# Optimization experiments

Hardware: AMD Instinct MI355X
Metric: run time of the kernel (lower is better)

The kernel has to match this reference:

```python
import jax, jax.numpy as jnp
from jax import lax
import numpy as np

_B, _D, _H, _W = 4, 32, 256, 256   # batch, sparse grid (z,y,x)
_NPER = 50000                      # active voxels per batch element
_EPS = 1e-3                        # BatchNorm eps from norm_fn


def _subm_rulebook(coords, D, H, W):
    # gather/scatter index pairs for a 3x3x3 submanifold conv (spconv rulebook)
    N = coords.shape[0]
    b, z, y, x = coords.T
    keys = ((b * D + z) * H + y) * W + x
    order = np.argsort(keys)
    sk = keys[order]
    rin, rout = [], []
    for dz in (-1, 0, 1):
        for dy in (-1, 0, 1):
            for dx in (-1, 0, 1):
                nz, ny, nx = z + dz, y + dy, x + dx
                valid = (nz >= 0) & (nz < D) & (ny >= 0) & (ny < H) & (nx >= 0) & (nx < W)
                qk = ((b * D + nz) * H + ny) * W + nx
                pos = np.clip(np.searchsorted(sk, qk), 0, N - 1)
                found = valid & (sk[pos] == qk)
                rin.append(order[pos[found]].astype(np.int32))
                rout.append(np.nonzero(found)[0].astype(np.int32))
    P = max(len(a) for a in rin)
    Ia = np.full((27, P), N, np.int32)   # sentinel N -> zero-padded row
    Oa = np.full((27, P), N, np.int32)
    for k in range(27):
        Ia[k, :len(rin[k])] = rin[k]
        Oa[k, :len(rout[k])] = rout[k]
    return Ia, Oa


def _build():
    rng = np.random.default_rng(0)
    coords = []
    for b in range(_B):
        lin = rng.choice(_D * _H * _W, _NPER, replace=False)
        z = lin // (_H * _W); y = (lin // _W) % _H; x = lin % _W
        coords.append(np.stack([np.full(_NPER, b), z, y, x], 1))
    coords = np.concatenate(coords).astype(np.int64)
    N = coords.shape[0]
    rb1_in, rb1_out = _subm_rulebook(coords, _D, _H, _W)
    # strided SparseConv3d (k=3, s=2, p=1) rulebook + output coord set
    Do, Ho, Wo = (_D - 1) // 2 + 1, (_H - 1) // 2 + 1, (_W - 1) // 2 + 1
    b, z, y, x = coords.T
    cin, ck, ckey = [], [], []
    k = 0
    for dz in range(3):
        for dy in range(3):
            for dx in range(3):
                oz2, oy2, ox2 = z + 1 - dz, y + 1 - dy, x + 1 - dx
                valid = (oz2 % 2 == 0) & (oy2 % 2 == 0) & (ox2 % 2 == 0)
                oz, oy, ox = oz2 // 2, oy2 // 2, ox2 // 2
                valid &= (oz >= 0) & (oz < Do) & (oy >= 0) & (oy < Ho) & (ox >= 0) & (ox < Wo)
                idx = np.nonzero(valid)[0]
                cin.append(idx)
                ck.append(np.full(len(idx), k))
                ckey.append(((b[idx] * Do + oz[idx]) * Ho + oy[idx]) * Wo + ox[idx])
                k += 1
    allkey = np.concatenate(ckey)
    ukeys, inv = np.unique(allkey, return_inverse=True)
    N2 = len(ukeys)
    cin = np.concatenate(cin); ck = np.concatenate(ck)
    Pd = max(int((ck == kk).sum()) for kk in range(27))
    Id = np.full((27, Pd), N, np.int32)
    Od = np.full((27, Pd), N2, np.int32)
    for kk in range(27):
        m = ck == kk; n = int(m.sum())
        Id[kk, :n] = cin[m]; Od[kk, :n] = inv[m]
    ox = ukeys % Wo; oy = (ukeys // Wo) % Ho
    oz = (ukeys // (Wo * Ho)) % Do; ob = ukeys // (Wo * Ho * Do)
    coords2 = np.stack([ob, oz, oy, ox], 1)
    rb2_in, rb2_out = _subm_rulebook(coords2, Do, Ho, Wo)
    return N, N2, rb1_in, rb1_out, Id, Od, rb2_in, rb2_out


def setup_inputs():
    N, N2, rb1_in, rb1_out, rbd_in, rbd_out, rb2_in, rb2_out = _build()
    ks = jax.random.split(jax.random.key(0), 8)
    Cin, C0, C1 = 5, 16, 32
    return dict(
        voxel_features=jax.random.normal(ks[0], (N, Cin), jnp.float32),
        W_in=jax.random.normal(ks[1], (27, Cin, C0), jnp.float32) * 0.1,
        g_in=jnp.ones(C0), b_in=jnp.zeros(C0),
        Wb1=jax.random.normal(ks[2], (2, 2, 27, C0, C0), jnp.float32) * 0.05,
        bb1=jnp.zeros((2, 2, C0)), gb1=jnp.ones((2, 2, C0)), beb1=jnp.zeros((2, 2, C0)),
        Wp=jax.random.normal(ks[3], (27, C0, 1), jnp.float32) * 0.05,
        Wd=jax.random.normal(ks[4], (27, C0, C1), jnp.float32) * 0.05,
        g_d=jnp.ones(C1), b_d=jnp.zeros(C1),
        Wb2=jax.random.normal(ks[5], (2, 2, 27, C1, C1), jnp.float32) * 0.05,
        bb2=jnp.zeros((2, 2, C1)), gb2=jnp.ones((2, 2, C1)), beb2=jnp.zeros((2, 2, C1)),
        rb1_in=jnp.asarray(rb1_in), rb1_out=jnp.asarray(rb1_out),
        rbd_in=jnp.asarray(rbd_in), rbd_out=jnp.asarray(rbd_out),
        rb2_in=jnp.asarray(rb2_in), rb2_out=jnp.asarray(rb2_out),
        n2=int(N2),
    )


def _sparse_conv(feat, W, rin, rout, nout):
    # rulebook gather-matmul-scatter; fixed 27-iteration loop over kernel offsets
    featp = jnp.concatenate([feat, jnp.zeros((1, feat.shape[1]), feat.dtype)], 0)
    out = jnp.zeros((nout + 1, W.shape[-1]), feat.dtype)
    for k in range(W.shape[0]):
        out = out.at[rout[k]].add(featp[rin[k]] @ W[k])
    return out[:nout]


def _bn(x, g, b):
    # training-mode BatchNorm1d over active voxels (eps=1e-3)
    m = x.mean(0)
    v = ((x - m) ** 2).mean(0)
    return g * (x - m) * lax.rsqrt(v + _EPS) + b


def _basic_block(feat, Wb, bb, gb, beb, rin, rout, n):
    out = _sparse_conv(feat, Wb[0], rin, rout, n) + bb[0]
    out = jax.nn.relu(_bn(out, gb[0], beb[0]))
    out = _sparse_conv(out, Wb[1], rin, rout, n) + bb[1]
    out = _bn(out, gb[1], beb[1])
    return jax.nn.relu(out + feat)


def _forward(voxel_features, W_in, g_in, b_in, Wb1, bb1, gb1, beb1, Wp, Wd, g_d, b_d,
             Wb2, bb2, gb2, beb2, rb1_in, rb1_out, rbd_in, rbd_out, rb2_in, rb2_out, n2):
    n1 = voxel_features.shape[0]
    # conv_input: SubMConv3d + BN + ReLU
    x = jax.nn.relu(_bn(_sparse_conv(voxel_features, W_in, rb1_in, rb1_out, n1), g_in, b_in))
    for i in range(2):
        x = _basic_block(x, Wb1[i], bb1[i], gb1[i], beb1[i], rb1_in, rb1_out, n1)
    # DynamicFocalPruningDownsample: learnable importance -> topk keep (1-0.5)
    imp = jax.nn.sigmoid(_sparse_conv(x, Wp, rb1_in, rb1_out, n1))[:, 0]
    x = x * imp[:, None]
    kkeep = n1 - n1 // 2
    kth = lax.top_k(imp, kkeep)[0][-1]
    x = jnp.where(imp[:, None] >= kth, x, jnp.zeros_like(x))
    # strided SparseConv3d 16->32 + BN + ReLU
    x2 = jax.nn.relu(_bn(_sparse_conv(x, Wd, rbd_in, rbd_out, n2), g_d, b_d))
    for i in range(2):
        x2 = _basic_block(x2, Wb2[i], bb2[i], gb2[i], beb2[i], rb2_in, rb2_out, n2)
    return x2


def reference(voxel_features, W_in, g_in, b_in, Wb1, bb1, gb1, beb1, Wp, Wd, g_d, b_d,
              Wb2, bb2, gb2, beb2, rb1_in, rb1_out, rbd_in, rbd_out, rb2_in, rb2_out, n2):
    return _forward(voxel_features, W_in, g_in, b_in, Wb1, bb1, gb1, beb1, Wp, Wd, g_d, b_d,
                    Wb2, bb2, gb2, beb2, rb1_in, rb1_out, rbd_in, rbd_out, rb2_in, rb2_out, n2)
```

## Files before the change

kernel.cpp:

```cpp
#include <hip/hip_runtime.h>


typedef __attribute__((ext_vector_type(8))) short bf16x8;
typedef __attribute__((ext_vector_type(4))) float f32x4;

static __device__ __forceinline__ unsigned f2bfu(float x) {
    unsigned b = __float_as_uint(x);
    return (b + 0x7FFFu + ((b >> 16) & 1u)) >> 16;
}
static __device__ __forceinline__ float bf2f(unsigned short u) {
    return __uint_as_float(((unsigned)u) << 16);
}
static __device__ __forceinline__ int xcd_swz(int bid, int nwg) {
    if (nwg < 16) return bid;
    int q = nwg >> 3, r = nwg & 7;
    int x = bid & 7, i = bid >> 3;
    return (x < r ? x * (q + 1) : r * (q + 1) + (x - r) * q) + i;
}

__global__ void rb_count_kernel(const int* __restrict__ rout, int P, int n_out,
                                int* __restrict__ cnt) {
    int k = threadIdx.x;
    if (k >= 27) return;
    const int* r = rout + (size_t)k * P;
    int lo = 0, hi = P;
    while (lo < hi) {
        int mid = (lo + hi) >> 1;
        if (r[mid] < n_out) lo = mid + 1; else hi = mid;
    }
    cnt[k] = lo;
}

__global__ void seg_build(const int* __restrict__ rout, const int* __restrict__ cnt,
                          int P, int nb, int gran, int* __restrict__ segs) {
    const int k = blockIdx.y;
    const int b = blockIdx.x * 256 + threadIdx.x;
    if (b > nb) return;
    const int target = b * gran;
    const int* r = rout + (size_t)k * P;
    int lo = 0, hi = cnt[k];
    while (lo < hi) {
        int m = (lo + hi) >> 1;
        if (r[m] < target) lo = m + 1; else hi = m;
    }
    segs[k * (nb + 1) + b] = lo;
}

__global__ void inv_build(const int* __restrict__ rin, const int* __restrict__ rout,
                          const int* __restrict__ cnt, int P, int n_out,
                          int* __restrict__ inv) {
    const int k = blockIdx.y;
    const int p = blockIdx.x * 256 + threadIdx.x;
    if (p < cnt[k])
        inv[(size_t)k * n_out + rout[(size_t)k * P + p]] = rin[(size_t)k * P + p];
}

__global__ void prepack_w(const float* __restrict__ W, int T, int CI, int S,
                          short* __restrict__ pack) {
    int idx = blockIdx.x * 256 + threadIdx.x;
    if (idx >= S * 128) return;
    int l = idx & 63, h = (idx >> 6) & 1, s = idx >> 7;
    int co = (l & 15) + 16 * h;
#pragma unroll
    for (int j = 0; j < 8; j++) {
        int gk = s * 32 + (l >> 4) * 8 + j;
        int tap = gk / CI, cin = gk % CI;
        float w = (tap < T) ? W[((size_t)tap * CI + cin) * 32 + co] : 0.f;
        pack[(size_t)idx * 8 + j] = (short)f2bfu(w);
    }
}

template <bool OUT_BF16>
__global__ __launch_bounds__(256, 4) void conv_mfma_inv32(
        const unsigned short* __restrict__ feat, const short* __restrict__ Bp,
        const int* __restrict__ inv, int n_out,
        void* __restrict__ outv, float* __restrict__ stats) {
    __shared__ float part[2][4][32];
    const int t = threadIdx.x, wv = t >> 6, lane = t & 63;
    const int row = lane & 15, grp = lane >> 4;
    const int bid = xcd_swz(blockIdx.x, gridDim.x);
    float ss0 = 0.f, qq0 = 0.f, ss1 = 0.f, qq1 = 0.f;

    for (int tile = 0; tile < 4; ++tile) {
        const int rowbase = bid * 256 + wv * 64 + tile * 16;
        if (rowbase >= n_out) break;
        const int j = rowbase + row;
        const bool jv = j < n_out;
        f32x4 d0 = {0.f, 0.f, 0.f, 0.f}, d1 = {0.f, 0.f, 0.f, 0.f};
#pragma unroll
        for (int k = 0; k < 27; ++k) {
            const int rn = jv ? inv[(size_t)k * n_out + j] : -1;
            union { int u[4]; bf16x8 v; } ua;
            ua.u[0] = ua.u[1] = ua.u[2] = ua.u[3] = 0;
            if (rn >= 0)
                ua.v = *(const bf16x8*)(feat + (size_t)rn * 32 + grp * 8);
            const bf16x8 b0 = *(const bf16x8*)(Bp + ((size_t)(2 * k) * 64 + lane) * 8);
            const bf16x8 b1 = *(const bf16x8*)(Bp + ((size_t)(2 * k + 1) * 64 + lane) * 8);
            d0 = __builtin_amdgcn_mfma_f32_16x16x32_bf16(ua.v, b0, d0, 0, 0, 0);
            d1 = __builtin_amdgcn_mfma_f32_16x16x32_bf16(ua.v, b1, d1, 0, 0, 0);
        }
        const int m0 = rowbase + grp * 4;
#pragma unroll
        for (int i = 0; i < 4; i++) {
            if (m0 + i < n_out) {
                if (OUT_BF16) {
                    unsigned short* o = (unsigned short*)outv;
                    o[(size_t)(m0 + i) * 32 + row]      = (unsigned short)f2bfu(d0[i]);
                    o[(size_t)(m0 + i) * 32 + row + 16] = (unsigned short)f2bfu(d1[i]);
                } else {
                    float* o = (float*)outv;
                    o[(size_t)(m0 + i) * 32 + row]      = d0[i];
                    o[(size_t)(m0 + i) * 32 + row + 16] = d1[i];
                }
            }
            ss0 += d0[i]; qq0 += d0[i] * d0[i];
            ss1 += d1[i]; qq1 += d1[i] * d1[i];
        }
    }
#pragma unroll
    for (int d = 16; d <= 32; d <<= 1) {
        ss0 += __shfl_xor(ss0, d); qq0 += __shfl_xor(qq0, d);
        ss1 += __shfl_xor(ss1, d); qq1 += __shfl_xor(qq1, d);
    }
    if (lane < 16) {
        part[0][wv][row] = ss0; part[0][wv][row + 16] = ss1;
        part[1][wv][row] = qq0; part[1][wv][row + 16] = qq1;
    }
    __syncthreads();
    if (t < 64) {
        const int which = t >> 5, co = t & 31;
        atomicAdd(&stats[which * 32 + co],
                  part[which][0][co] + part[which][1][co] +
                  part[which][2][co] + part[which][3][co]);
    }
}

__global__ __launch_bounds__(256, 4) void conv_mfma_inv16(
        const unsigned short* __restrict__ feat, const short* __restrict__ Bp,
        const int* __restrict__ inv, int n_out,
        unsigned short* __restrict__ out, float* __restrict__ stats) {
    __shared__ float part[2][4][32];
    const int t = threadIdx.x, wv = t >> 6, lane = t & 63;
    const int row = lane & 15, grp = lane >> 4;
    const int bid = xcd_swz(blockIdx.x, gridDim.x);
    float ss0 = 0.f, qq0 = 0.f, ss1 = 0.f, qq1 = 0.f;

    for (int tile = 0; tile < 4; ++tile) {
        const int rowbase = bid * 256 + wv * 64 + tile * 16;
        if (rowbase >= n_out) break;
        const int j = rowbase + row;
        const bool jv = j < n_out;
        f32x4 d0 = {0.f, 0.f, 0.f, 0.f}, d1 = {0.f, 0.f, 0.f, 0.f};
#pragma unroll
        for (int s = 0; s < 14; ++s) {
            const int tap = 2 * s + (grp >> 1);
            const int cin0 = (grp & 1) * 8;
            int rn = -1;
            if (tap < 27 && jv) rn = inv[(size_t)tap * n_out + j];
            union { int u[4]; bf16x8 v; } ua;
            ua.u[0] = ua.u[1] = ua.u[2] = ua.u[3] = 0;
            if (rn >= 0)
                ua.v = *(const bf16x8*)(feat + (size_t)rn * 16 + cin0);
            const bf16x8 b0 = *(const bf16x8*)(Bp + ((size_t)(2 * s) * 64 + lane) * 8);
            const bf16x8 b1 = *(const bf16x8*)(Bp + ((size_t)(2 * s + 1) * 64 + lane) * 8);
            d0 = __builtin_amdgcn_mfma_f32_16x16x32_bf16(ua.v, b0, d0, 0, 0, 0);
            d1 = __builtin_amdgcn_mfma_f32_16x16x32_bf16(ua.v, b1, d1, 0, 0, 0);
        }
        const int m0 = rowbase + grp * 4;
#pragma unroll
        for (int i = 0; i < 4; i++) {
            if (m0 + i < n_out) {
                out[(size_t)(m0 + i) * 32 + row]      = (unsigned short)f2bfu(d0[i]);
                out[(size_t)(m0 + i) * 32 + row + 16] = (unsigned short)f2bfu(d1[i]);
            }
            ss0 += d0[i]; qq0 += d0[i] * d0[i];
            ss1 += d1[i]; qq1 += d1[i] * d1[i];
        }
    }
#pragma unroll
    for (int d = 16; d <= 32; d <<= 1) {
        ss0 += __shfl_xor(ss0, d); qq0 += __shfl_xor(qq0, d);
        ss1 += __shfl_xor(ss1, d); qq1 += __shfl_xor(qq1, d);
    }
    if (lane < 16) {
        part[0][wv][row] = ss0; part[0][wv][row + 16] = ss1;
        part[1][wv][row] = qq0; part[1][wv][row + 16] = qq1;
    }
    __syncthreads();
    if (t < 64) {
        const int which = t >> 5, co = t & 31;
        atomicAdd(&stats[which * 32 + co],
                  part[which][0][co] + part[which][1][co] +
                  part[which][2][co] + part[which][3][co]);
    }
}

template <int COUT, bool SIGMOID, bool STATS>
__global__ __launch_bounds__(256) void conv16_wave(
        const float* __restrict__ feat, const float* __restrict__ W,
        const int* __restrict__ rin, const int* __restrict__ rout,
        const int* __restrict__ segs, int P, int nb64, int n_out,
        float* __restrict__ out, float* __restrict__ stats) {
    __shared__ int invw[4 * 64];
    __shared__ float part[2][4][COUT];
    const int t = threadIdx.x, wv = t >> 6, lane = t & 63;
    const int bid = xcd_swz(blockIdx.x, gridDim.x);
    const int rowbase = bid * 256 + wv * 64;
    const bool active = rowbase < n_out;
    float acc[COUT];
#pragma unroll
    for (int co = 0; co < COUT; co++) acc[co] = 0.f;

    if (active) {
        const int tix = rowbase >> 6;
        int segv = 0;
        if (lane < 28)      segv = segs[lane * (nb64 + 1) + tix];
        else if (lane < 56) segv = segs[(lane - 28) * (nb64 + 1) + tix + 1];
        for (int k = 0; k < 27; ++k) {
            const int s0 = __shfl(segv, k);
            const int s1 = __shfl(segv, 28 + k);
            if (s0 == s1) continue;
            invw[wv * 64 + lane] = -1;
            const int e = s0 + lane;
            if (e < s1)
                invw[wv * 64 + (rout[(size_t)k * P + e] - rowbase)] = rin[(size_t)k * P + e];
            asm volatile("s_waitcnt lgkmcnt(0)" ::: "memory");
            const int rn = invw[wv * 64 + lane];
            float f[16];
#pragma unroll
            for (int ci = 0; ci < 16; ci++) f[ci] = 0.f;
            if (rn >= 0) {
                const float* fr = feat + (size_t)rn * 16;
#pragma unroll
                for (int q = 0; q < 4; q++) {
                    const float4 v = *(const float4*)(fr + 4 * q);
                    f[4 * q] = v.x; f[4 * q + 1] = v.y;
                    f[4 * q + 2] = v.z; f[4 * q + 3] = v.w;
                }
            }
            const float* __restrict__ Wk = W + k * 16 * COUT;
#pragma unroll
            for (int ci = 0; ci < 16; ci++) {
                const float fv = f[ci];
#pragma unroll
                for (int co = 0; co < COUT; co++)
                    acc[co] = fmaf(fv, Wk[ci * COUT + co], acc[co]);
            }
        }
        const int j = rowbase + lane;
        if (j < n_out) {
#pragma unroll
            for (int co = 0; co < COUT; co++) {
                float v = acc[co];
                if (SIGMOID) v = 1.f / (1.f + expf(-v));
                out[(size_t)j * COUT + co] = v;
            }
        }
    }
    if (STATS) {
#pragma unroll
        for (int co = 0; co < COUT; co++) {
            float s = acc[co], s2 = s * s;
#pragma unroll
            for (int d = 1; d < 64; d <<= 1) {
                s += __shfl_xor(s, d);
                s2 += __shfl_xor(s2, d);
            }
            if (lane == 0) { part[0][wv][co] = s; part[1][wv][co] = s2; }
        }
        __syncthreads();
        if (t < 2 * COUT) {
            const int which = t / COUT, co = t - which * COUT;
            atomicAdd(&stats[which * COUT + co],
                      part[which][0][co] + part[which][1][co] +
                      part[which][2][co] + part[which][3][co]);
        }
    }
}

template <int CIN, int COUT>
__global__ __launch_bounds__(256) void conv_gather(
        const float* __restrict__ feat, const float* __restrict__ W,
        const int* __restrict__ rin, const int* __restrict__ rout,
        const int* __restrict__ segs, int P, int n_out,
        float* __restrict__ out, float* __restrict__ stats) {
    __shared__ int2 invl[256];
    __shared__ int seg[54];
    __shared__ float part[2][4][COUT];
    const int t = threadIdx.x;
    const int bid = xcd_swz(blockIdx.x, gridDim.x);
    const int j0 = bid * 256;
    const int nb1 = gridDim.x + 1;
    if (t < 54) seg[t] = segs[(t >> 1) * nb1 + bid + (t & 1)];
    invl[t] = make_int2(-1, -1);
    float acc[COUT];
#pragma unroll
    for (int co = 0; co < COUT; co++) acc[co] = 0.f;
    __syncthreads();

    for (int k = 0; k < 27; k++) {
        const int s0 = seg[2 * k], s1 = seg[2 * k + 1];
        if (s0 == s1) continue;
        const int idx = s0 + t;
        if (idx < s1)
            invl[rout[(size_t)k * P + idx] - j0] = make_int2(k, rin[(size_t)k * P + idx]);
        __syncthreads();
        const int2 e = invl[t];
        const int in = (e.x == k) ? e.y : -1;
        __syncthreads();

        float f[CIN];
#pragma unroll
        for (int ci = 0; ci < CIN; ci++) f[ci] = 0.f;
        if (in >= 0) {
            const float* fr = feat + (size_t)in * CIN;
#pragma unroll
            for (int ci = 0; ci < CIN; ci++) f[ci] = fr[ci];
        }
        const float* __restrict__ Wk = W + k * CIN * COUT;
#pragma unroll
        for (int ci = 0; ci < CIN; ci++) {
            const float fv = f[ci];
#pragma unroll
            for (int co = 0; co < COUT; co++)
                acc[co] = fmaf(fv, Wk[ci * COUT + co], acc[co]);
        }
    }

    const int j = j0 + t;
    if (j < n_out) {
#pragma unroll
        for (int co = 0; co < COUT; co++) out[(size_t)j * COUT + co] = acc[co];
    }
    const int wv = t >> 6, lane = t & 63;
#pragma unroll
    for (int co = 0; co < COUT; co++) {
        float s = acc[co], s2 = s * s;
#pragma unroll
        for (int d = 1; d < 64; d <<= 1) {
            s += __shfl_xor(s, d);
            s2 += __shfl_xor(s2, d);
        }
        if (lane == 0) { part[0][wv][co] = s; part[1][wv][co] = s2; }
    }
    __syncthreads();
    if (t < 2 * COUT) {
        const int which = t / COUT, co = t - which * COUT;
        atomicAdd(&stats[which * COUT + co],
                  part[which][0][co] + part[which][1][co] +
                  part[which][2][co] + part[which][3][co]);
    }
}

template <int C, bool RELU>
__global__ void bn_apply(const float* __restrict__ x, const float* __restrict__ stats,
                         const float* __restrict__ gg, const float* __restrict__ bb,
                         int n, float* __restrict__ y) {
    const float nf = (float)n;
    const long long total = (long long)n * C;
    for (long long idx = (long long)blockIdx.x * blockDim.x + threadIdx.x;
         idx < total; idx += (long long)gridDim.x * blockDim.x) {
        int ch = (int)(idx & (C - 1));
        float m = stats[ch] / nf;
        float v = stats[C + ch] / nf - m * m;
        float r = rsqrtf(v + 1e-3f);
        float val = gg[ch] * (x[idx] - m) * r + bb[ch];
        if (RELU) val = fmaxf(val, 0.f);
        y[idx] = val;
    }
}

template <int C>
__global__ void bn_apply_addrelu(const float* __restrict__ x,
                                 const float* __restrict__ skip,
                                 const float* __restrict__ stats,
                                 const float* __restrict__ gg,
                                 const float* __restrict__ bb,
                                 int n, float* __restrict__ y) {
    const float nf = (float)n;
    const long long total = (long long)n * C;
    for (long long idx = (long long)blockIdx.x * blockDim.x + threadIdx.x;
         idx < total; idx += (long long)gridDim.x * blockDim.x) {
        int ch = (int)(idx & (C - 1));
        float m = stats[ch] / nf;
        float v = stats[C + ch] / nf - m * m;
        float r = rsqrtf(v + 1e-3f);
        float val = gg[ch] * (x[idx] - m) * r + bb[ch] + skip[idx];
        y[idx] = fmaxf(val, 0.f);
    }
}

template <int C>
__global__ void bn_apply_b(const unsigned short* __restrict__ x,
                           const float* __restrict__ stats,
                           const float* __restrict__ gg, const float* __restrict__ bb,
                           int n, unsigned short* __restrict__ y) {
    const float nf = (float)n;
    const long long total = (long long)n * C;
    for (long long idx = (long long)blockIdx.x * blockDim.x + threadIdx.x;
         idx < total; idx += (long long)gridDim.x * blockDim.x) {
        int ch = (int)(idx & (C - 1));
        float m = stats[ch] / nf;
        float v = stats[C + ch] / nf - m * m;
        float r = rsqrtf(v + 1e-3f);
        float val = gg[ch] * (bf2f(x[idx]) - m) * r + bb[ch];
        val = fmaxf(val, 0.f);
        y[idx] = (unsigned short)f2bfu(val);
    }
}

template <int C, bool XBF16, bool OUT_BF16>
__global__ void bn_addrelu_x(const void* __restrict__ xv,
                             const unsigned short* __restrict__ skip,
                             const float* __restrict__ stats,
                             const float* __restrict__ gg,
                             const float* __restrict__ bb,
                             int n, void* __restrict__ yv) {
    const float nf = (float)n;
    const long long total = (long long)n * C;
    for (long long idx = (long long)blockIdx.x * blockDim.x + threadIdx.x;
         idx < total; idx += (long long)gridDim.x * blockDim.x) {
        int ch = (int)(idx & (C - 1));
        float m = stats[ch] / nf;
        float v = stats[C + ch] / nf - m * m;
        float r = rsqrtf(v + 1e-3f);
        float x = XBF16 ? bf2f(((const unsigned short*)xv)[idx])
                        : ((const float*)xv)[idx];
        float val = gg[ch] * (x - m) * r + bb[ch] + bf2f(skip[idx]);
        val = fmaxf(val, 0.f);
        if (OUT_BF16) ((unsigned short*)yv)[idx] = (unsigned short)f2bfu(val);
        else          ((float*)yv)[idx] = val;
    }
}

__global__ __launch_bounds__(256) void hist_pass(const float* __restrict__ imp, int n,
                                                 int pass, const int* __restrict__ state,
                                                 int* __restrict__ hist) {
    __shared__ int lh[256];
    const int t = threadIdx.x;
    lh[t] = 0;
    __syncthreads();
    const int shift = 24 - 8 * pass;
    unsigned prefix = 0;
    if (pass > 0) prefix = (unsigned)state[0];
    for (int i = blockIdx.x * 256 + t; i < n; i += gridDim.x * 256) {
        unsigned u = __float_as_uint(imp[i]);
        if (pass == 0 || (u >> (shift + 8)) == prefix)
            atomicAdd(&lh[(u >> shift) & 0xFFu], 1);
    }
    __syncthreads();
    if (lh[t]) atomicAdd(&hist[pass * 256 + t], lh[t]);
}

__global__ __launch_bounds__(256) void scan_byte(const int* __restrict__ hist,
                                                 int kkeep, int pass,
                                                 int* __restrict__ state) {
    __shared__ int h[256];
    const int t = threadIdx.x;
    h[t] = hist[pass * 256 + t];
    __syncthreads();
    if (t == 0) {
        const int target = (pass == 0) ? kkeep : state[1];
        int acc = 0; int b = 255;
        for (; b > 0; b--) {
            if (acc + h[b] >= target) break;
            acc += h[b];
        }
        unsigned prefix = (pass == 0) ? 0u : (unsigned)state[0];
        prefix = (prefix << 8) | (unsigned)b;
        state[0] = (int)prefix;
        state[1] = target - acc;
        if (pass == 3) state[2] = (int)prefix;
    }
}

__global__ void prune_mask_ab(const float* __restrict__ x, const float* __restrict__ imp,
                              const int* __restrict__ state, int n,
                              unsigned short* __restrict__ ab) {
    const unsigned K = (unsigned)state[2];
    int i = blockIdx.x * blockDim.x + threadIdx.x;
    if (i >= n) return;
    float im = imp[i];
    float mult = (__float_as_uint(im) >= K) ? im : 0.f;
#pragma unroll
    for (int c = 0; c < 16; c++)
        ab[(size_t)i * 16 + c] = (unsigned short)f2bfu(x[(size_t)i * 16 + c] * mult);
}

extern "C" void kernel_launch(void* const* d_in, const int* in_sizes, int n_in,
                              void* d_out, int out_size, void* d_ws, size_t ws_size,
                              hipStream_t stream) {
    const float* vf    = (const float*)d_in[0];
    const float* W_in  = (const float*)d_in[1];
    const float* g_in  = (const float*)d_in[2];
    const float* b_in  = (const float*)d_in[3];
    const float* Wb1   = (const float*)d_in[4];
    const float* gb1   = (const float*)d_in[6];
    const float* beb1  = (const float*)d_in[7];
    const float* Wp    = (const float*)d_in[8];
    const float* Wd    = (const float*)d_in[9];
    const float* g_d   = (const float*)d_in[10];
    const float* b_d   = (const float*)d_in[11];
    const float* Wb2   = (const float*)d_in[12];
    const float* gb2   = (const float*)d_in[14];
    const float* beb2  = (const float*)d_in[15];
    const int* rb1_in  = (const int*)d_in[16];
    const int* rb1_out = (const int*)d_in[17];
    const int* rbd_in  = (const int*)d_in[18];
    const int* rbd_out = (const int*)d_in[19];
    const int* rb2_in  = (const int*)d_in[20];
    const int* rb2_out = (const int*)d_in[21];

    const int N  = in_sizes[0] / 5;
    const int P1 = in_sizes[16] / 27;
    const int Pd = in_sizes[18] / 27;
    const int P2 = in_sizes[20] / 27;
    const int n2 = out_size / 32;
    const int kkeep = N - N / 2;

    const int gs1   = (N + 255) / 256;
    const int gm2   = (n2 + 255) / 256;
    const int nb64  = (N + 63) / 64;
    const int gew   = 2048;

    auto pad4 = [](size_t v) { return (v + 3) & ~(size_t)3; };
    float* A     = (float*)d_ws;
    float* B     = A   + pad4((size_t)N * 16);
    float* imp   = B   + pad4((size_t)N * 16);
    float* INVf  = imp + pad4((size_t)N);
    float* Dbf   = INVf + pad4((size_t)n2 * 27);
    float* Ebf   = Dbf + pad4((size_t)n2 * 16);
    float* stats = Ebf + pad4((size_t)n2 * 16);
    int*   cnt1  = (int*)(stats + 64);
    int*   cntd  = cnt1 + 32;
    int*   cnt2  = cntd + 32;
    int*   hist4 = cnt2 + 32;
    int*   state = hist4 + 1024;
    int*   segs1 = state + 8;
    int*   segs64 = segs1 + 27 * (gs1 + 1);
    int*   INV    = (int*)INVf;
    unsigned short* Ab = (unsigned short*)B;
    short* pack2  = (short*)imp;
    short* packd  = pack2 + 4 * 27648;
    unsigned short* Db = (unsigned short*)Dbf;
    unsigned short* Eb = (unsigned short*)Ebf;
    float* OUT   = (float*)d_out;
    unsigned short* OUTb = (unsigned short*)d_out;
    float* C2    = OUT;

    rb_count_kernel<<<1, 32, 0, stream>>>(rb1_out, P1, N,  cnt1);
    rb_count_kernel<<<1, 32, 0, stream>>>(rbd_out, Pd, n2, cntd);
    rb_count_kernel<<<1, 32, 0, stream>>>(rb2_out, P2, n2, cnt2);
    seg_build<<<dim3((gs1 + 256) / 256, 27), 256, 0, stream>>>(rb1_out, cnt1, P1, gs1, 256, segs1);
    seg_build<<<dim3((nb64 + 256) / 256, 27), 256, 0, stream>>>(rb1_out, cnt1, P1, nb64, 64, segs64);

    hipMemsetAsync(stats, 0, 64 * 4, stream);
    conv_gather<5, 16><<<gs1, 256, 0, stream>>>(vf, W_in, rb1_in, rb1_out, segs1, P1, N, B, stats);
    bn_apply<16, true><<<gew, 256, 0, stream>>>(B, stats, g_in, b_in, N, A);

    for (int i = 0; i < 2; i++) {
        const float* W0 = Wb1 + (size_t)(i * 2 + 0) * 27 * 256;
        const float* W1 = Wb1 + (size_t)(i * 2 + 1) * 27 * 256;
        hipMemsetAsync(stats, 0, 64 * 4, stream);
        conv16_wave<16, false, true><<<gs1, 256, 0, stream>>>(A, W0, rb1_in, rb1_out, segs64, P1, nb64, N, B, stats);
        bn_apply<16, true><<<gew, 256, 0, stream>>>(B, stats, gb1 + (i * 2 + 0) * 16, beb1 + (i * 2 + 0) * 16, N, B);
        hipMemsetAsync(stats, 0, 64 * 4, stream);
        conv16_wave<16, false, true><<<gs1, 256, 0, stream>>>(B, W1, rb1_in, rb1_out, segs64, P1, nb64, N, C2, stats);
        bn_apply_addrelu<16><<<gew, 256, 0, stream>>>(C2, A, stats, gb1 + (i * 2 + 1) * 16, beb1 + (i * 2 + 1) * 16, N, A);
    }

    conv16_wave<1, true, false><<<gs1, 256, 0, stream>>>(A, Wp, rb1_in, rb1_out, segs64, P1, nb64, N, imp, stats);
    hipMemsetAsync(hist4, 0, 1024 * 4, stream);
    for (int p = 0; p < 4; p++) {
        hist_pass<<<128, 256, 0, stream>>>(imp, N, p, state, hist4);
        scan_byte<<<1, 256, 0, stream>>>(hist4, kkeep, p, state);
    }
    prune_mask_ab<<<(N + 255) / 256, 256, 0, stream>>>(A, imp, state, N, Ab);

    for (int w = 0; w < 4; w++)
        prepack_w<<<14, 256, 0, stream>>>(Wb2 + (size_t)w * 27 * 1024, 27, 32, 27, pack2 + (size_t)w * 27648);
    prepack_w<<<7, 256, 0, stream>>>(Wd, 27, 16, 14, packd);
    hipMemsetAsync(INV, 0xFF, (size_t)27 * n2 * 4, stream);
    inv_build<<<dim3((Pd + 255) / 256, 27), 256, 0, stream>>>(rbd_in, rbd_out, cntd, Pd, n2, INV);

    hipMemsetAsync(stats, 0, 64 * 4, stream);
    conv_mfma_inv16<<<gm2, 256, 0, stream>>>(Ab, packd, INV, n2, Db, stats);
    bn_apply_b<32><<<gew, 256, 0, stream>>>(Db, stats, g_d, b_d, n2, Db);

    hipMemsetAsync(INV, 0xFF, (size_t)27 * n2 * 4, stream);
    inv_build<<<dim3((P2 + 255) / 256, 27), 256, 0, stream>>>(rb2_in, rb2_out, cnt2, P2, n2, INV);

    for (int i = 0; i < 2; i++) {
        const short* P0 = pack2 + (size_t)(i * 2 + 0) * 27648;
        const short* P1w = pack2 + (size_t)(i * 2 + 1) * 27648;
        hipMemsetAsync(stats, 0, 64 * 4, stream);
        conv_mfma_inv32<true><<<gm2, 256, 0, stream>>>(Db, P0, INV, n2, Eb, stats);
        bn_apply_b<32><<<gew, 256, 0, stream>>>(Eb, stats, gb2 + (i * 2 + 0) * 32, beb2 + (i * 2 + 0) * 32, n2, Eb);
        hipMemsetAsync(stats, 0, 64 * 4, stream);
        if (i == 0) {
            conv_mfma_inv32<true><<<gm2, 256, 0, stream>>>(Eb, P1w, INV, n2, OUTb, stats);
            bn_addrelu_x<32, true, true><<<gew, 256, 0, stream>>>(OUTb, Db, stats, gb2 + 32, beb2 + 32, n2, Db);
        } else {
            conv_mfma_inv32<false><<<gm2, 256, 0, stream>>>(Eb, P1w, INV, n2, OUT, stats);
            bn_addrelu_x<32, false, false><<<gew, 256, 0, stream>>>(OUT, Db, stats, gb2 + 96, beb2 + 96, n2, OUT);
        }
    }
}
```

Measured before the change: 1.580 ms.

## Use dense inverse index tables for level-1 convs and branchless zero-row gathers

Replaces the segment-based, shared-memory scatter approach in the 16-channel level-1 convolutions with a dense per-tap inverse index table built once via inv_build. Every thread now does a flat 27-tap gather. All gathers become branchless by pointing invalid or missing neighbours at an appended zero row, which each feature buffer now reserves and clears. The MFMA kernels also drop the 4-waves occupancy hint from their launch bounds. This removes per-tap segment lookups, LDS writes and divergent branches, in exchange for an extra index-table build, a larger INV allocation and unconditional loads of the zero row.

```diff
diff --git a/kernel.cpp b/kernel.cpp
--- a/kernel.cpp
+++ b/kernel.cpp
@@ -71,7 +71,7 @@
 }
 
 template <bool OUT_BF16>
-__global__ __launch_bounds__(256, 4) void conv_mfma_inv32(
+__global__ __launch_bounds__(256) void conv_mfma_inv32(
         const unsigned short* __restrict__ feat, const short* __restrict__ Bp,
         const int* __restrict__ inv, int n_out,
         void* __restrict__ outv, float* __restrict__ stats) {
@@ -85,15 +85,15 @@
         const int rowbase = bid * 256 + wv * 64 + tile * 16;
         if (rowbase >= n_out) break;
         const int j = rowbase + row;
+        const int jm = min(j, n_out - 1);
         const bool jv = j < n_out;
         f32x4 d0 = {0.f, 0.f, 0.f, 0.f}, d1 = {0.f, 0.f, 0.f, 0.f};
 #pragma unroll
         for (int k = 0; k < 27; ++k) {
-            const int rn = jv ? inv[(size_t)k * n_out + j] : -1;
+            int rn = inv[(size_t)k * n_out + jm];
+            rn = (jv && rn >= 0) ? rn : n_out;
             union { int u[4]; bf16x8 v; } ua;
-            ua.u[0] = ua.u[1] = ua.u[2] = ua.u[3] = 0;
-            if (rn >= 0)
-                ua.v = *(const bf16x8*)(feat + (size_t)rn * 32 + grp * 8);
+            ua.v = *(const bf16x8*)(feat + (size_t)rn * 32 + grp * 8);
             const bf16x8 b0 = *(const bf16x8*)(Bp + ((size_t)(2 * k) * 64 + lane) * 8);
             const bf16x8 b1 = *(const bf16x8*)(Bp + ((size_t)(2 * k + 1) * 64 + lane) * 8);
             d0 = __builtin_amdgcn_mfma_f32_16x16x32_bf16(ua.v, b0, d0, 0, 0, 0);
@@ -135,9 +135,9 @@
     }
 }
 
-__global__ __launch_bounds__(256, 4) void conv_mfma_inv16(
+__global__ __launch_bounds__(256) void conv_mfma_inv16(
         const unsigned short* __restrict__ feat, const short* __restrict__ Bp,
-        const int* __restrict__ inv, int n_out,
+        const int* __restrict__ inv, int n_out, int nzero,
         unsigned short* __restrict__ out, float* __restrict__ stats) {
     __shared__ float part[2][4][32];
     const int t = threadIdx.x, wv = t >> 6, lane = t & 63;
@@ -149,18 +149,18 @@
         const int rowbase = bid * 256 + wv * 64 + tile * 16;
         if (rowbase >= n_out) break;
         const int j = rowbase + row;
+        const int jm = min(j, n_out - 1);
         const bool jv = j < n_out;
         f32x4 d0 = {0.f, 0.f, 0.f, 0.f}, d1 = {0.f, 0.f, 0.f, 0.f};
 #pragma unroll
         for (int s = 0; s < 14; ++s) {
             const int tap = 2 * s + (grp >> 1);
             const int cin0 = (grp & 1) * 8;
-            int rn = -1;
-            if (tap < 27 && jv) rn = inv[(size_t)tap * n_out + j];
+            const int tapc = min(tap, 26);
+            int rn = inv[(size_t)tapc * n_out + jm];
+            rn = (jv && tap < 27 && rn >= 0) ? rn : nzero;
             union { int u[4]; bf16x8 v; } ua;
-            ua.u[0] = ua.u[1] = ua.u[2] = ua.u[3] = 0;
-            if (rn >= 0)
-                ua.v = *(const bf16x8*)(feat + (size_t)rn * 16 + cin0);
+            ua.v = *(const bf16x8*)(feat + (size_t)rn * 16 + cin0);
             const bf16x8 b0 = *(const bf16x8*)(Bp + ((size_t)(2 * s) * 64 + lane) * 8);
             const bf16x8 b1 = *(const bf16x8*)(Bp + ((size_t)(2 * s + 1) * 64 + lane) * 8);
             d0 = __builtin_amdgcn_mfma_f32_16x16x32_bf16(ua.v, b0, d0, 0, 0, 0);
@@ -196,65 +196,47 @@
 }
 
 template <int COUT, bool SIGMOID, bool STATS>
-__global__ __launch_bounds__(256) void conv16_wave(
+__global__ __launch_bounds__(256) void conv16f_inv(
         const float* __restrict__ feat, const float* __restrict__ W,
-        const int* __restrict__ rin, const int* __restrict__ rout,
-        const int* __restrict__ segs, int P, int nb64, int n_out,
+        const int* __restrict__ inv, int n_out, int nzero,
         float* __restrict__ out, float* __restrict__ stats) {
-    __shared__ int invw[4 * 64];
     __shared__ float part[2][4][COUT];
     const int t = threadIdx.x, wv = t >> 6, lane = t & 63;
     const int bid = xcd_swz(blockIdx.x, gridDim.x);
-    const int rowbase = bid * 256 + wv * 64;
-    const bool active = rowbase < n_out;
+    const int j = bid * 256 + t;
+    const int jm = min(j, n_out - 1);
+    const bool jv = j < n_out;
     float acc[COUT];
 #pragma unroll
     for (int co = 0; co < COUT; co++) acc[co] = 0.f;
 
-    if (active) {
-        const int tix = rowbase >> 6;
-        int segv = 0;
-        if (lane < 28)      segv = segs[lane * (nb64 + 1) + tix];
-        else if (lane < 56) segv = segs[(lane - 28) * (nb64 + 1) + tix + 1];
-        for (int k = 0; k < 27; ++k) {
-            const int s0 = __shfl(segv, k);
-            const int s1 = __shfl(segv, 28 + k);
-            if (s0 == s1) continue;
-            invw[wv * 64 + lane] = -1;
-            const int e = s0 + lane;
-            if (e < s1)
-                invw[wv * 64 + (rout[(size_t)k * P + e] - rowbase)] = rin[(size_t)k * P + e];
-            asm volatile("s_waitcnt lgkmcnt(0)" ::: "memory");
-            const int rn = invw[wv * 64 + lane];
-            float f[16];
-#pragma unroll
-            for (int ci = 0; ci < 16; ci++) f[ci] = 0.f;
-            if (rn >= 0) {
-                const float* fr = feat + (size_t)rn * 16;
-#pragma unroll
-                for (int q = 0; q < 4; q++) {
-                    const float4 v = *(const float4*)(fr + 4 * q);
-                    f[4 * q] = v.x; f[4 * q + 1] = v.y;
-                    f[4 * q + 2] = v.z; f[4 * q + 3] = v.w;
-                }
-            }
-            const float* __restrict__ Wk = W + k * 16 * COUT;
-#pragma unroll
-            for (int ci = 0; ci < 16; ci++) {
-                const float fv = f[ci];
-#pragma unroll
-                for (int co = 0; co < COUT; co++)
-                    acc[co] = fmaf(fv, Wk[ci * COUT + co], acc[co]);
-            }
-        }
-        const int j = rowbase + lane;
-        if (j < n_out) {
-#pragma unroll
-            for (int co = 0; co < COUT; co++) {
-                float v = acc[co];
-                if (SIGMOID) v = 1.f / (1.f + expf(-v));
-                out[(size_t)j * COUT + co] = v;
-            }
+#pragma unroll
+    for (int k = 0; k < 27; ++k) {
+        int rn = inv[(size_t)k * n_out + jm];
+        rn = (jv && rn >= 0) ? rn : nzero;
+        const float* fr = feat + (size_t)rn * 16;
+        float f[16];
+#pragma unroll
+        for (int q = 0; q < 4; q++) {
+            const float4 v = *(const float4*)(fr + 4 * q);
+            f[4 * q] = v.x; f[4 * q + 1] = v.y;
+            f[4 * q + 2] = v.z; f[4 * q + 3] = v.w;
+        }
+        const float* __restrict__ Wk = W + k * 16 * COUT;
+#pragma unroll
+        for (int ci = 0; ci < 16; ci++) {
+            const float fv = f[ci];
+#pragma unroll
+            for (int co = 0; co < COUT; co++)
+                acc[co] = fmaf(fv, Wk[ci * COUT + co], acc[co]);
+        }
+    }
+    if (jv) {
+#pragma unroll
+        for (int co = 0; co < COUT; co++) {
+            float v = acc[co];
+            if (SIGMOID) v = 1.f / (1.f + expf(-v));
+            out[(size_t)j * COUT + co] = v;
         }
     }
     if (STATS) {
@@ -517,27 +499,26 @@
     const int P2 = in_sizes[20] / 27;
     const int n2 = out_size / 32;
     const int kkeep = N - N / 2;
+    const int nInv = (N > n2) ? N : n2;
 
     const int gs1   = (N + 255) / 256;
     const int gm2   = (n2 + 255) / 256;
-    const int nb64  = (N + 63) / 64;
     const int gew   = 2048;
 
     auto pad4 = [](size_t v) { return (v + 3) & ~(size_t)3; };
     float* A     = (float*)d_ws;
-    float* B     = A   + pad4((size_t)N * 16);
-    float* imp   = B   + pad4((size_t)N * 16);
+    float* B     = A   + pad4((size_t)N * 16 + 16);
+    float* imp   = B   + pad4((size_t)N * 16 + 16);
     float* INVf  = imp + pad4((size_t)N);
-    float* Dbf   = INVf + pad4((size_t)n2 * 27);
-    float* Ebf   = Dbf + pad4((size_t)n2 * 16);
-    float* stats = Ebf + pad4((size_t)n2 * 16);
+    float* Dbf   = INVf + pad4((size_t)nInv * 27);
+    float* Ebf   = Dbf + pad4((size_t)n2 * 16 + 16);
+    float* stats = Ebf + pad4((size_t)n2 * 16 + 16);
     int*   cnt1  = (int*)(stats + 64);
     int*   cntd  = cnt1 + 32;
     int*   cnt2  = cntd + 32;
     int*   hist4 = cnt2 + 32;
     int*   state = hist4 + 1024;
     int*   segs1 = state + 8;
-    int*   segs64 = segs1 + 27 * (gs1 + 1);
     int*   INV    = (int*)INVf;
     unsigned short* Ab = (unsigned short*)B;
     short* pack2  = (short*)imp;
@@ -552,7 +533,11 @@
     rb_count_kernel<<<1, 32, 0, stream>>>(rbd_out, Pd, n2, cntd);
     rb_count_kernel<<<1, 32, 0, stream>>>(rb2_out, P2, n2, cnt2);
     seg_build<<<dim3((gs1 + 256) / 256, 27), 256, 0, stream>>>(rb1_out, cnt1, P1, gs1, 256, segs1);
-    seg_build<<<dim3((nb64 + 256) / 256, 27), 256, 0, stream>>>(rb1_out, cnt1, P1, nb64, 64, segs64);
+
+    hipMemsetAsync(INV, 0xFF, (size_t)27 * N * 4, stream);
+    inv_build<<<dim3((P1 + 255) / 256, 27), 256, 0, stream>>>(rb1_in, rb1_out, cnt1, P1, N, INV);
+    hipMemsetAsync(A + (size_t)N * 16, 0, 64, stream);
+    hipMemsetAsync(B + (size_t)N * 16, 0, 64, stream);
 
     hipMemsetAsync(stats, 0, 64 * 4, stream);
     conv_gather<5, 16><<<gs1, 256, 0, stream>>>(vf, W_in, rb1_in, rb1_out, segs1, P1, N, B, stats);
@@ -562,14 +547,14 @@
         const float* W0 = Wb1 + (size_t)(i * 2 + 0) * 27 * 256;
         const float* W1 = Wb1 + (size_t)(i * 2 + 1) * 27 * 256;
         hipMemsetAsync(stats, 0, 64 * 4, stream);
-        conv16_wave<16, false, true><<<gs1, 256, 0, stream>>>(A, W0, rb1_in, rb1_out, segs64, P1, nb64, N, B, stats);
+        conv16f_inv<16, false, true><<<gs1, 256, 0, stream>>>(A, W0, INV, N, N, B, stats);
         bn_apply<16, true><<<gew, 256, 0, stream>>>(B, stats, gb1 + (i * 2 + 0) * 16, beb1 + (i * 2 + 0) * 16, N, B);
         hipMemsetAsync(stats, 0, 64 * 4, stream);
-        conv16_wave<16, false, true><<<gs1, 256, 0, stream>>>(B, W1, rb1_in, rb1_out, segs64, P1, nb64, N, C2, stats);
+        conv16f_inv<16, false, true><<<gs1, 256, 0, stream>>>(B, W1, INV, N, N, C2, stats);
         bn_apply_addrelu<16><<<gew, 256, 0, stream>>>(C2, A, stats, gb1 + (i * 2 + 1) * 16, beb1 + (i * 2 + 1) * 16, N, A);
     }
 
-    conv16_wave<1, true, false><<<gs1, 256, 0, stream>>>(A, Wp, rb1_in, rb1_out, segs64, P1, nb64, N, imp, stats);
+    conv16f_inv<1, true, false><<<gs1, 256, 0, stream>>>(A, Wp, INV, N, N, imp, stats);
     hipMemsetAsync(hist4, 0, 1024 * 4, stream);
     for (int p = 0; p < 4; p++) {
         hist_pass<<<128, 256, 0, stream>>>(imp, N, p, state, hist4);
@@ -580,11 +565,14 @@
     for (int w = 0; w < 4; w++)
         prepack_w<<<14, 256, 0, stream>>>(Wb2 + (size_t)w * 27 * 1024, 27, 32, 27, pack2 + (size_t)w * 27648);
     prepack_w<<<7, 256, 0, stream>>>(Wd, 27, 16, 14, packd);
+    hipMemsetAsync((char*)Ab + (size_t)N * 32, 0, 32, stream);
+    hipMemsetAsync((char*)Db + (size_t)n2 * 64, 0, 64, stream);
+    hipMemsetAsync((char*)Eb + (size_t)n2 * 64, 0, 64, stream);
     hipMemsetAsync(INV, 0xFF, (size_t)27 * n2 * 4, stream);
     inv_build<<<dim3((Pd + 255) / 256, 27), 256, 0, stream>>>(rbd_in, rbd_out, cntd, Pd, n2, INV);
 
     hipMemsetAsync(stats, 0, 64 * 4, stream);
-    conv_mfma_inv16<<<gm2, 256, 0, stream>>>(Ab, packd, INV, n2, Db, stats);
+    conv_mfma_inv16<<<gm2, 256, 0, stream>>>(Ab, packd, INV, n2, N, Db, stats);
     bn_apply_b<32><<<gew, 256, 0, stream>>>(Db, stats, g_d, b_d, n2, Db);
 
     hipMemsetAsync(INV, 0xFF, (size_t)27 * n2 * 4, stream);
```

Result: slower. 1.660 ms (+5.1%).
